# Kernel optimization log

Hardware: AMD Instinct MI355X
Metric: run time of the kernel (lower is better)

Reference implementation:

```python
import jax, jax.numpy as jnp
import numpy as np

INPUT, HIDDEN, CLASSES = 4096, 4096, 1000


def setup_inputs() -> dict:
    key = jax.random.key(0)
    kx, kw1, kb1, kw2, kb2 = jax.random.split(key, 5)
    return {
        "x": jax.random.normal(kx, (8192, INPUT), dtype=jnp.float32),
        "fc1_weight": jax.random.normal(kw1, (HIDDEN, INPUT), dtype=jnp.float32),
        "fc1_bias": jax.random.normal(kb1, (HIDDEN,), dtype=jnp.float32),
        "fc2_weight": jax.random.normal(kw2, (CLASSES, HIDDEN), dtype=jnp.float32),
        "fc2_bias": jax.random.normal(kb2, (CLASSES,), dtype=jnp.float32),
    }


def reference(x, fc1_weight, fc1_bias, fc2_weight, fc2_bias):
    # x: [B, INPUT] (module flattens; already flat here)
    hidden = jnp.einsum("bi,hi->bh", x, fc1_weight) + fc1_bias  # [B, H]
    activated = jax.nn.relu(hidden)
    logits = jnp.einsum("bh,ch->bc", activated, fc2_weight) + fc2_bias  # [B, C]
    return jax.nn.softmax(logits, axis=-1)
```

## Files before the change

kernel.cpp:

```cpp
#include <hip/hip_runtime.h>
#include <hip/hip_fp16.h>
#include <stdint.h>

typedef __attribute__((ext_vector_type(8)))  _Float16 f16x8;
typedef __attribute__((ext_vector_type(4)))  _Float16 f16x4;
typedef __attribute__((ext_vector_type(4)))  float    f32x4;

__device__ __forceinline__ void split4(const f32x4 v, f16x4 &h, f16x4 &l) {
    #pragma unroll
    for (int i = 0; i < 4; ++i) {
        float a = v[i];
        _Float16 hh = (_Float16)a;
        h[i] = hh;
        l[i] = (_Float16)(a - (float)hh);
    }
}

__global__ __launch_bounds__(256)
void split_rows(const float* __restrict__ src, _Float16* __restrict__ h,
                _Float16* __restrict__ l, int srcRows, long long total4)
{
    const long long stride = (long long)gridDim.x * blockDim.x;
    for (long long i = (long long)blockIdx.x * blockDim.x + threadIdx.x; i < total4; i += stride) {
        const long long e = i << 2;
        const int row = (int)(e >> 12);
        f16x4 hv = {}, lv = {};
        if (row < srcRows) {
            f32x4 v = *(const f32x4*)(src + e);
            split4(v, hv, lv);
        }
        *(f16x4*)(h + e) = hv;
        *(f16x4*)(l + e) = lv;
    }
}


#define BARRIER() __builtin_amdgcn_s_barrier()
#define SB0()     __builtin_amdgcn_sched_barrier(0)
#define MFMA16    __builtin_amdgcn_mfma_f32_16x16x32_f16
#define SGB       __builtin_amdgcn_sched_group_barrier

template<int N> __device__ __forceinline__ void VMCNT() {
    asm volatile("s_waitcnt vmcnt(%0)" :: "n"(N) : "memory");
    __builtin_amdgcn_sched_barrier(0);
}

__device__ __forceinline__ void gload16(const _Float16* g, _Float16* l) {
    __builtin_amdgcn_global_load_lds(
        (const __attribute__((address_space(1))) void*)g,
        (__attribute__((address_space(3))) void*)l, 16, 0, 0);
}

template<int MI, bool SPLITOUT, bool CHUNKSWZ>
__global__ __launch_bounds__(512, 2)
void gemm3_v9(const _Float16* __restrict__ Agh, const _Float16* __restrict__ Agl,
              const _Float16* __restrict__ Bgh, const _Float16* __restrict__ Bgl,
              const float* __restrict__ bias,
              _Float16* __restrict__ Oh, _Float16* __restrict__ Ol,
              float* __restrict__ Of, int ldo, int Nstore,
              int K, int nBN)
{
    extern __shared__ _Float16 lds[];
    constexpr int WROWS = MI * 16;
    constexpr int BM    = MI * 32;
    constexpr int CHA   = MI * 2;
    constexpr int PW    = (2*CHA + 32) / 8;
    constexpr int H1    = PW - CHA/8;
    constexpr int H2    = CHA / 8;
    constexpr int ALO   = CHA * 512;
    constexpr int BHO   = 2 * CHA * 512;
    constexpr int BUFS  = 2*CHA*512 + 16384;

    const int tid  = threadIdx.x;
    const int lane = tid & 63;
    const int wave = tid >> 6;
    const int wm = wave >> 2;
    const int wn = wave & 3;
    const int fr = lane & 15;
    const int fg = lane >> 4;

    int bm, bn;
    const int orig = blockIdx.x;
    if (CHUNKSWZ) {
        bm = ((orig & 7) << 2) | ((orig >> 3) & 3);
        bn = orig >> 5;
    } else {
        const int cpx  = gridDim.x >> 3;
        const int swzb = (orig & 7) * cpx + (orig >> 3);
        bn = swzb % nBN;
        bm = swzb / nBN;
    }
    const int m0 = bm * BM;
    const int n0 = bn * 256;

    const _Float16* gptr[8];
    int loff[8];
    #pragma unroll
    for (int i = 0; i < PW; ++i) {
        int p, q;
        if (i < H2 || i >= H1) {
            const bool hi = (i >= H1);
            const int  s  = hi ? (i - H1) : i;
            const int  j  = wave * H2 + s;
            p = j / (CHA / 2);
            const int v   = j % (CHA / 2);
            const int wmq = v / (MI / 2);
            const int wi  = v % (MI / 2);
            q = wmq * MI + (hi ? MI / 2 : 0) + wi;
        } else {
            q = (i - H2) + (wave & 3) * 4;
            p = 2 + (wave >> 2);
        }
        const int row = q*16 + (lane >> 2);
        const int gc  = (lane & 3) ^ ((row >> 1) & 3);
        const _Float16* plane = (p == 0) ? Agh : (p == 1) ? Agl : (p == 2) ? Bgh : Bgl;
        const size_t grow = (size_t)((p < 2) ? m0 : n0) + row;
        gptr[i] = plane + grow * (size_t)K + gc * 8;
        loff[i] = ((p < 2) ? p * ALO : BHO + (p - 2) * 8192) + q * 512;
    }

    const int swz8 = (fg ^ ((fr >> 1) & 3)) * 8;
    int aoff[MI], boff[4];
    #pragma unroll
    for (int mi = 0; mi < MI; ++mi) aoff[mi] = (wm*WROWS + mi*16 + fr)*32 + swz8;
    #pragma unroll
    for (int ni = 0; ni < 4; ++ni)  boff[ni] = BHO + (wn*64 + ni*16 + fr)*32 + swz8;

    f32x4 acc[MI][4] = {};

    #pragma unroll
    for (int i = 0; i < PW; ++i) { gload16(gptr[i], &lds[loff[i]]); gptr[i] += 32; }
    VMCNT<0>(); BARRIER(); SB0();

    const int NT = K >> 5;
    int bb = 0;

#define MFMA3(NI, AH, AL) do {                                           \
        acc[0][NI] = MFMA16((AH), bh##NI, acc[0][NI], 0, 0, 0);          \
        acc[0][NI] = MFMA16((AH), bl##NI, acc[0][NI], 0, 0, 0);          \
        acc[0][NI] = MFMA16((AL), bh##NI, acc[0][NI], 0, 0, 0);          \
    } while (0)

#define MFMA12(MIdx, AH, AL) do {                                        \
        acc[MIdx][0] = MFMA16((AH), bh0, acc[MIdx][0], 0, 0, 0);         \
        acc[MIdx][1] = MFMA16((AH), bh1, acc[MIdx][1], 0, 0, 0);         \
        acc[MIdx][2] = MFMA16((AH), bh2, acc[MIdx][2], 0, 0, 0);         \
        acc[MIdx][3] = MFMA16((AH), bh3, acc[MIdx][3], 0, 0, 0);         \
        acc[MIdx][0] = MFMA16((AH), bl0, acc[MIdx][0], 0, 0, 0);         \
        acc[MIdx][1] = MFMA16((AH), bl1, acc[MIdx][1], 0, 0, 0);         \
        acc[MIdx][2] = MFMA16((AH), bl2, acc[MIdx][2], 0, 0, 0);         \
        acc[MIdx][3] = MFMA16((AH), bl3, acc[MIdx][3], 0, 0, 0);         \
        acc[MIdx][0] = MFMA16((AL), bh0, acc[MIdx][0], 0, 0, 0);         \
        acc[MIdx][1] = MFMA16((AL), bh1, acc[MIdx][1], 0, 0, 0);         \
        acc[MIdx][2] = MFMA16((AL), bh2, acc[MIdx][2], 0, 0, 0);         \
        acc[MIdx][3] = MFMA16((AL), bh3, acc[MIdx][3], 0, 0, 0);         \
    } while (0)

#define STEP_BODY(STG)                                                            \
    do {                                                                          \
        if (STG) {                                                                \
            _Pragma("unroll")                                                     \
            for (int i = 0; i < PW; ++i) {                                        \
                gload16(gptr[i], &lds[nbuf + loff[i]]); gptr[i] += 32;            \
            }                                                                     \
        }                                                                         \
        f16x8 ah[2], al[2];                                                       \
        f16x8 bh0, bl0, bh1, bl1, bh2, bl2, bh3, bl3;                             \
        ah[0] = *(const f16x8*)&lds[bb + aoff[0]];                                \
        al[0] = *(const f16x8*)&lds[bb + ALO + aoff[0]];                          \
        bh0 = *(const f16x8*)&lds[bb + boff[0]];                                  \
        bl0 = *(const f16x8*)&lds[bb + 8192 + boff[0]];                           \
        if (STG) SGB(0x010, PW, 0);                                               \
        SGB(0x100, 4, 0);                                                         \
        MFMA3(0, ah[0], al[0]);                                                   \
        SGB(0x008, 3, 0);                                                         \
        bh1 = *(const f16x8*)&lds[bb + boff[1]];                                  \
        bl1 = *(const f16x8*)&lds[bb + 8192 + boff[1]];                           \
        SGB(0x100, 2, 0);                                                         \
        MFMA3(1, ah[0], al[0]);                                                   \
        SGB(0x008, 3, 0);                                                         \
        bh2 = *(const f16x8*)&lds[bb + boff[2]];                                  \
        bl2 = *(const f16x8*)&lds[bb + 8192 + boff[2]];                           \
        SGB(0x100, 2, 0);                                                         \
        MFMA3(2, ah[0], al[0]);                                                   \
        SGB(0x008, 3, 0);                                                         \
        bh3 = *(const f16x8*)&lds[bb + boff[3]];                                  \
        bl3 = *(const f16x8*)&lds[bb + 8192 + boff[3]];                           \
        ah[1] = *(const f16x8*)&lds[bb + aoff[1]];                                \
        al[1] = *(const f16x8*)&lds[bb + ALO + aoff[1]];                          \
        SGB(0x100, 4, 0);                                                         \
        MFMA3(3, ah[0], al[0]);                                                   \
        SGB(0x008, 3, 0);                                                         \
        _Pragma("unroll")                                                         \
        for (int mi = 1; mi < MI; ++mi) {                                         \
            if (mi < MI - 1) {                                                    \
                ah[(mi + 1) & 1] = *(const f16x8*)&lds[bb + aoff[mi + 1]];        \
                al[(mi + 1) & 1] = *(const f16x8*)&lds[bb + ALO + aoff[mi + 1]];  \
                SGB(0x100, 2, 0);                                                 \
            }                                                                     \
            MFMA12(mi, ah[mi & 1], al[mi & 1]);                                   \
            SGB(0x008, 12, 0);                                                    \
        }                                                                         \
    } while (0)

    for (int t = 0; t < NT - 1; ++t) {
        const int nbuf = BUFS - bb;
        STEP_BODY(true);
        VMCNT<0>(); BARRIER(); SB0();
        bb = nbuf;
    }
    {
        const int nbuf = 0; (void)nbuf;
        STEP_BODY(false);
    }
#undef STEP_BODY
#undef MFMA12
#undef MFMA3

    #pragma unroll
    for (int ni = 0; ni < 4; ++ni) {
        const int n = n0 + wn*64 + ni*16 + fr;
        if (!SPLITOUT && n >= Nstore) continue;
        const float bv = bias[n];
        #pragma unroll
        for (int mi = 0; mi < MI; ++mi) {
            #pragma unroll
            for (int j = 0; j < 4; ++j) {
                const int m = m0 + wm*WROWS + mi*16 + fg*4 + j;
                float v = acc[mi][ni][j] + bv;
                if (SPLITOUT) {
                    v = fmaxf(v, 0.f);
                    const _Float16 hh = (_Float16)v;
                    Oh[(size_t)m * ldo + n] = hh;
                    Ol[(size_t)m * ldo + n] = (_Float16)(v - (float)hh);
                } else {
                    Of[(size_t)m * ldo + n] = v;
                }
            }
        }
    }
}

#define TILE_M 128
#define TILE_N 128
#define TILE_K 32
#define LDSK   40

template<bool RELU, bool NGUARD>
__global__ __launch_bounds__(256, 2)
void gemm_split3(const float* __restrict__ A, const float* __restrict__ B,
                 const float* __restrict__ bias, float* __restrict__ C,
                 int K, int ldc, int Nreal)
{
    __shared__ _Float16 Ah[TILE_M][LDSK];
    __shared__ _Float16 Al[TILE_M][LDSK];
    __shared__ _Float16 Bh[TILE_N][LDSK];
    __shared__ _Float16 Bl[TILE_N][LDSK];

    const int tid  = threadIdx.x;
    const int lane = tid & 63;
    const int wave = tid >> 6;
    const int wr   = wave >> 1;
    const int wc   = wave & 1;
    const int m0   = blockIdx.x * TILE_M;
    const int n0   = blockIdx.y * TILE_N;
    const int srow = tid >> 3;
    const int scol = (tid & 7) << 2;
    const int fr = lane & 15;
    const int fg = lane >> 4;

    f32x4 acc[4][4] = {};

    for (int kt = 0; kt < K; kt += TILE_K) {
        __syncthreads();
        #pragma unroll
        for (int p = 0; p < 4; ++p) {
            const int row = srow + p * 32;
            f32x4 v = *(const f32x4*)(A + (size_t)(m0 + row) * K + kt + scol);
            f16x4 hv, lv;
            split4(v, hv, lv);
            *(f16x4*)&Ah[row][scol] = hv;
            *(f16x4*)&Al[row][scol] = lv;
        }
        #pragma unroll
        for (int p = 0; p < 4; ++p) {
            const int row = srow + p * 32;
            f32x4 v = {0.f, 0.f, 0.f, 0.f};
            if (!NGUARD || (n0 + row) < Nreal)
                v = *(const f32x4*)(B + (size_t)(n0 + row) * K + kt + scol);
            f16x4 hv, lv;
            split4(v, hv, lv);
            *(f16x4*)&Bh[row][scol] = hv;
            *(f16x4*)&Bl[row][scol] = lv;
        }
        __syncthreads();

        f16x8 ah[4], al[4];
        #pragma unroll
        for (int mi = 0; mi < 4; ++mi) {
            const int r = wr * 64 + mi * 16 + fr;
            ah[mi] = *(const f16x8*)&Ah[r][fg * 8];
            al[mi] = *(const f16x8*)&Al[r][fg * 8];
        }
        #pragma unroll
        for (int ni = 0; ni < 4; ++ni) {
            const int r = wc * 64 + ni * 16 + fr;
            const f16x8 bh = *(const f16x8*)&Bh[r][fg * 8];
            const f16x8 bl = *(const f16x8*)&Bl[r][fg * 8];
            #pragma unroll
            for (int mi = 0; mi < 4; ++mi) {
                acc[mi][ni] = __builtin_amdgcn_mfma_f32_16x16x32_f16(ah[mi], bh, acc[mi][ni], 0, 0, 0);
                acc[mi][ni] = __builtin_amdgcn_mfma_f32_16x16x32_f16(ah[mi], bl, acc[mi][ni], 0, 0, 0);
                acc[mi][ni] = __builtin_amdgcn_mfma_f32_16x16x32_f16(al[mi], bh, acc[mi][ni], 0, 0, 0);
            }
        }
    }

    #pragma unroll
    for (int ni = 0; ni < 4; ++ni) {
        const int n = n0 + wc * 64 + ni * 16 + fr;
        if (NGUARD && n >= Nreal) continue;
        const float bv = bias[n];
        #pragma unroll
        for (int mi = 0; mi < 4; ++mi) {
            #pragma unroll
            for (int j = 0; j < 4; ++j) {
                const int m = m0 + wr * 64 + mi * 16 + fg * 4 + j;
                float val = acc[mi][ni][j] + bv;
                if (RELU) val = fmaxf(val, 0.f);
                C[(size_t)m * ldc + n] = val;
            }
        }
    }
}

__global__ __launch_bounds__(256)
void softmax_rows(float* __restrict__ out, int rows, int cols)
{
    const int lane = threadIdx.x & 63;
    const int row  = blockIdx.x * 4 + (threadIdx.x >> 6);
    if (row >= rows) return;
    float* p = out + (size_t)row * cols;

    float v[16];
    float mx = -3.4e38f;
    #pragma unroll
    for (int j = 0; j < 16; ++j) {
        const int c = lane + j * 64;
        v[j] = (c < cols) ? p[c] : -3.4e38f;
        mx = fmaxf(mx, v[j]);
    }
    #pragma unroll
    for (int off = 32; off > 0; off >>= 1)
        mx = fmaxf(mx, __shfl_xor(mx, off));

    float s = 0.f;
    #pragma unroll
    for (int j = 0; j < 16; ++j) {
        const int c = lane + j * 64;
        const float e = (c < cols) ? __expf(v[j] - mx) : 0.f;
        v[j] = e;
        s += e;
    }
    #pragma unroll
    for (int off = 32; off > 0; off >>= 1)
        s += __shfl_xor(s, off);

    const float inv = 1.f / s;
    #pragma unroll
    for (int j = 0; j < 16; ++j) {
        const int c = lane + j * 64;
        if (c < cols) p[c] = v[j] * inv;
    }
}

extern "C" void kernel_launch(void* const* d_in, const int* in_sizes, int n_in,
                              void* d_out, int out_size, void* d_ws, size_t ws_size,
                              hipStream_t stream)
{
    const float* x  = (const float*)d_in[0];
    const float* w1 = (const float*)d_in[1];
    const float* b1 = (const float*)d_in[2];
    const float* w2 = (const float*)d_in[3];
    const float* b2 = (const float*)d_in[4];
    float* out = (float*)d_out;

    const size_t SZ_X  = (size_t)8192 * 4096 * 2;
    const size_t SZ_W1 = (size_t)4096 * 4096 * 2;
    const size_t SZ_W2 = (size_t)1024 * 4096 * 2;

    size_t off = 0;
    auto take = [&](size_t b) { size_t o = off; off += (b + 255) & ~(size_t)255; return o; };
    const size_t o_xh  = take(SZ_X),  o_xl  = take(SZ_X);
    const size_t o_w1h = take(SZ_W1), o_w1l = take(SZ_W1);
    const size_t o_w2h = take(SZ_W2), o_w2l = take(SZ_W2);
    const size_t o_ah  = take(SZ_X),  o_al  = take(SZ_X);
    const size_t need = off;

    bool attr_ok =
        (hipFuncSetAttribute((const void*)gemm3_v9<8, true, true>,
                             hipFuncAttributeMaxDynamicSharedMemorySize, 131072) == hipSuccess) &&
        (hipFuncSetAttribute((const void*)gemm3_v9<4, false, false>,
                             hipFuncAttributeMaxDynamicSharedMemorySize, 131072) == hipSuccess);

    const dim3 blk256(256, 1, 1), blk512(512, 1, 1);

    if (attr_ok && ws_size >= need) {
        char* w = (char*)d_ws;
        _Float16 *xh  = (_Float16*)(w + o_xh),  *xl  = (_Float16*)(w + o_xl);
        _Float16 *w1h = (_Float16*)(w + o_w1h), *w1l = (_Float16*)(w + o_w1l);
        _Float16 *w2h = (_Float16*)(w + o_w2h), *w2l = (_Float16*)(w + o_w2l);
        _Float16 *ath = (_Float16*)(w + o_ah),  *atl = (_Float16*)(w + o_al);

        hipLaunchKernelGGL(split_rows, dim3(2048), blk256, 0, stream, x,  xh,  xl,  8192, (long long)8192 * 1024);
        hipLaunchKernelGGL(split_rows, dim3(2048), blk256, 0, stream, w1, w1h, w1l, 4096, (long long)4096 * 1024);
        hipLaunchKernelGGL(split_rows, dim3(1024), blk256, 0, stream, w2, w2h, w2l, 1000, (long long)1024 * 1024);

        hipLaunchKernelGGL((gemm3_v9<8, true, true>), dim3(512), blk512, 131072, stream,
                           xh, xl, w1h, w1l, b1, ath, atl, (float*)nullptr, 4096, 4096, 4096, 16);
        hipLaunchKernelGGL((gemm3_v9<4, false, false>), dim3(256), blk512, 98304, stream,
                           ath, atl, w2h, w2l, b2, (_Float16*)nullptr, (_Float16*)nullptr,
                           out, 1000, 1000, 4096, 4);
        hipLaunchKernelGGL(softmax_rows, dim3(2048), blk256, 0, stream, out, 8192, 1000);
    } else {
        float* act = (float*)d_ws;
        hipLaunchKernelGGL((gemm_split3<true, false>), dim3(64, 32), blk256, 0, stream,
                           x, w1, b1, act, 4096, 4096, 4096);
        hipLaunchKernelGGL((gemm_split3<false, true>), dim3(64, 8), blk256, 0, stream,
                           act, w2, b2, out, 4096, 1000, 1000);
        hipLaunchKernelGGL(softmax_rows, dim3(2048), blk256, 0, stream, out, 8192, 1000);
    }
}
```

Before: 953.5 us.

## Shrink GEMM block tile to 128x128 with smaller LDS for higher occupancy

```diff
diff --git a/kernel.cpp b/kernel.cpp
--- a/kernel.cpp
+++ b/kernel.cpp
@@ -51,25 +51,20 @@
         (__attribute__((address_space(3))) void*)l, 16, 0, 0);
 }
 
-template<int MI, bool SPLITOUT, bool CHUNKSWZ>
-__global__ __launch_bounds__(512, 2)
-void gemm3_v9(const _Float16* __restrict__ Agh, const _Float16* __restrict__ Agl,
-              const _Float16* __restrict__ Bgh, const _Float16* __restrict__ Bgl,
-              const float* __restrict__ bias,
-              _Float16* __restrict__ Oh, _Float16* __restrict__ Ol,
-              float* __restrict__ Of, int ldo, int Nstore,
-              int K, int nBN)
+template<bool SPLITOUT>
+__global__ __launch_bounds__(512, 4)
+void gemm3_v10(const _Float16* __restrict__ Agh, const _Float16* __restrict__ Agl,
+               const _Float16* __restrict__ Bgh, const _Float16* __restrict__ Bgl,
+               const float* __restrict__ bias,
+               _Float16* __restrict__ Oh, _Float16* __restrict__ Ol,
+               float* __restrict__ Of, int ldo, int Nstore,
+               int K)
 {
     extern __shared__ _Float16 lds[];
-    constexpr int WROWS = MI * 16;
-    constexpr int BM    = MI * 32;
-    constexpr int CHA   = MI * 2;
-    constexpr int PW    = (2*CHA + 32) / 8;
-    constexpr int H1    = PW - CHA/8;
-    constexpr int H2    = CHA / 8;
-    constexpr int ALO   = CHA * 512;
-    constexpr int BHO   = 2 * CHA * 512;
-    constexpr int BUFS  = 2*CHA*512 + 16384;
+    constexpr int PW   = 4;
+    constexpr int ALO  = 4096;
+    constexpr int BHO  = 8192;
+    constexpr int BUFS = 16384;
 
     const int tid  = threadIdx.x;
     const int lane = tid & 63;
@@ -79,54 +74,35 @@
     const int fr = lane & 15;
     const int fg = lane >> 4;
 
-    int bm, bn;
     const int orig = blockIdx.x;
-    if (CHUNKSWZ) {
-        bm = ((orig & 7) << 2) | ((orig >> 3) & 3);
-        bn = orig >> 5;
-    } else {
-        const int cpx  = gridDim.x >> 3;
-        const int swzb = (orig & 7) * cpx + (orig >> 3);
-        bn = swzb % nBN;
-        bm = swzb / nBN;
-    }
-    const int m0 = bm * BM;
-    const int n0 = bn * 256;
-
-    const _Float16* gptr[8];
-    int loff[8];
+    const int bm = ((orig & 7) << 3) | ((orig >> 3) & 7);
+    const int bn = orig >> 6;
+    const int m0 = bm * 128;
+    const int n0 = bn * 128;
+
+    const _Float16* gptr[PW];
+    int loff[PW];
     #pragma unroll
     for (int i = 0; i < PW; ++i) {
-        int p, q;
-        if (i < H2 || i >= H1) {
-            const bool hi = (i >= H1);
-            const int  s  = hi ? (i - H1) : i;
-            const int  j  = wave * H2 + s;
-            p = j / (CHA / 2);
-            const int v   = j % (CHA / 2);
-            const int wmq = v / (MI / 2);
-            const int wi  = v % (MI / 2);
-            q = wmq * MI + (hi ? MI / 2 : 0) + wi;
-        } else {
-            q = (i - H2) + (wave & 3) * 4;
-            p = 2 + (wave >> 2);
-        }
+        const int c = wave * PW + i;
+        const int p = c >> 3;
+        const int q = c & 7;
         const int row = q*16 + (lane >> 2);
         const int gc  = (lane & 3) ^ ((row >> 1) & 3);
         const _Float16* plane = (p == 0) ? Agh : (p == 1) ? Agl : (p == 2) ? Bgh : Bgl;
         const size_t grow = (size_t)((p < 2) ? m0 : n0) + row;
         gptr[i] = plane + grow * (size_t)K + gc * 8;
-        loff[i] = ((p < 2) ? p * ALO : BHO + (p - 2) * 8192) + q * 512;
+        loff[i] = p * 4096 + q * 512;
     }
 
     const int swz8 = (fg ^ ((fr >> 1) & 3)) * 8;
-    int aoff[MI], boff[4];
-    #pragma unroll
-    for (int mi = 0; mi < MI; ++mi) aoff[mi] = (wm*WROWS + mi*16 + fr)*32 + swz8;
-    #pragma unroll
-    for (int ni = 0; ni < 4; ++ni)  boff[ni] = BHO + (wn*64 + ni*16 + fr)*32 + swz8;
-
-    f32x4 acc[MI][4] = {};
+    int aoff[4], boff[2];
+    #pragma unroll
+    for (int mi = 0; mi < 4; ++mi) aoff[mi] = (wm*64 + mi*16 + fr)*32 + swz8;
+    #pragma unroll
+    for (int ni = 0; ni < 2; ++ni)  boff[ni] = BHO + (wn*32 + ni*16 + fr)*32 + swz8;
+
+    f32x4 acc[4][2] = {};
 
     #pragma unroll
     for (int i = 0; i < PW; ++i) { gload16(gptr[i], &lds[loff[i]]); gptr[i] += 32; }
@@ -135,25 +111,10 @@
     const int NT = K >> 5;
     int bb = 0;
 
-#define MFMA3(NI, AH, AL) do {                                           \
-        acc[0][NI] = MFMA16((AH), bh##NI, acc[0][NI], 0, 0, 0);          \
-        acc[0][NI] = MFMA16((AH), bl##NI, acc[0][NI], 0, 0, 0);          \
-        acc[0][NI] = MFMA16((AL), bh##NI, acc[0][NI], 0, 0, 0);          \
-    } while (0)
-
-#define MFMA12(MIdx, AH, AL) do {                                        \
-        acc[MIdx][0] = MFMA16((AH), bh0, acc[MIdx][0], 0, 0, 0);         \
-        acc[MIdx][1] = MFMA16((AH), bh1, acc[MIdx][1], 0, 0, 0);         \
-        acc[MIdx][2] = MFMA16((AH), bh2, acc[MIdx][2], 0, 0, 0);         \
-        acc[MIdx][3] = MFMA16((AH), bh3, acc[MIdx][3], 0, 0, 0);         \
-        acc[MIdx][0] = MFMA16((AH), bl0, acc[MIdx][0], 0, 0, 0);         \
-        acc[MIdx][1] = MFMA16((AH), bl1, acc[MIdx][1], 0, 0, 0);         \
-        acc[MIdx][2] = MFMA16((AH), bl2, acc[MIdx][2], 0, 0, 0);         \
-        acc[MIdx][3] = MFMA16((AH), bl3, acc[MIdx][3], 0, 0, 0);         \
-        acc[MIdx][0] = MFMA16((AL), bh0, acc[MIdx][0], 0, 0, 0);         \
-        acc[MIdx][1] = MFMA16((AL), bh1, acc[MIdx][1], 0, 0, 0);         \
-        acc[MIdx][2] = MFMA16((AL), bh2, acc[MIdx][2], 0, 0, 0);         \
-        acc[MIdx][3] = MFMA16((AL), bh3, acc[MIdx][3], 0, 0, 0);         \
+#define MFMA3(MIdx, NIdx, AH, AL, BH, BL) do {                               \
+        acc[MIdx][NIdx] = MFMA16((AH), (BH), acc[MIdx][NIdx], 0, 0, 0);      \
+        acc[MIdx][NIdx] = MFMA16((AH), (BL), acc[MIdx][NIdx], 0, 0, 0);      \
+        acc[MIdx][NIdx] = MFMA16((AL), (BH), acc[MIdx][NIdx], 0, 0, 0);      \
     } while (0)
 
 #define STEP_BODY(STG)                                                            \
@@ -165,41 +126,33 @@
             }                                                                     \
         }                                                                         \
         f16x8 ah[2], al[2];                                                       \
-        f16x8 bh0, bl0, bh1, bl1, bh2, bl2, bh3, bl3;                             \
+        f16x8 bh0, bl0, bh1, bl1;                                                 \
         ah[0] = *(const f16x8*)&lds[bb + aoff[0]];                                \
         al[0] = *(const f16x8*)&lds[bb + ALO + aoff[0]];                          \
         bh0 = *(const f16x8*)&lds[bb + boff[0]];                                  \
-        bl0 = *(const f16x8*)&lds[bb + 8192 + boff[0]];                           \
+        bl0 = *(const f16x8*)&lds[bb + 4096 + boff[0]];                           \
         if (STG) SGB(0x010, PW, 0);                                               \
         SGB(0x100, 4, 0);                                                         \
-        MFMA3(0, ah[0], al[0]);                                                   \
+        MFMA3(0, 0, ah[0], al[0], bh0, bl0);                                      \
         SGB(0x008, 3, 0);                                                         \
         bh1 = *(const f16x8*)&lds[bb + boff[1]];                                  \
-        bl1 = *(const f16x8*)&lds[bb + 8192 + boff[1]];                           \
+        bl1 = *(const f16x8*)&lds[bb + 4096 + boff[1]];                           \
         SGB(0x100, 2, 0);                                                         \
-        MFMA3(1, ah[0], al[0]);                                                   \
+        MFMA3(0, 1, ah[0], al[0], bh1, bl1);                                      \
         SGB(0x008, 3, 0);                                                         \
-        bh2 = *(const f16x8*)&lds[bb + boff[2]];                                  \
-        bl2 = *(const f16x8*)&lds[bb + 8192 + boff[2]];                           \
-        SGB(0x100, 2, 0);                                                         \
-        MFMA3(2, ah[0], al[0]);                                                   \
-        SGB(0x008, 3, 0);                                                         \
-        bh3 = *(const f16x8*)&lds[bb + boff[3]];                                  \
-        bl3 = *(const f16x8*)&lds[bb + 8192 + boff[3]];                           \
         ah[1] = *(const f16x8*)&lds[bb + aoff[1]];                                \
         al[1] = *(const f16x8*)&lds[bb + ALO + aoff[1]];                          \
-        SGB(0x100, 4, 0);                                                         \
-        MFMA3(3, ah[0], al[0]);                                                   \
-        SGB(0x008, 3, 0);                                                         \
+        SGB(0x100, 2, 0);                                                         \
         _Pragma("unroll")                                                         \
-        for (int mi = 1; mi < MI; ++mi) {                                         \
-            if (mi < MI - 1) {                                                    \
+        for (int mi = 1; mi < 4; ++mi) {                                          \
+            if (mi < 3) {                                                         \
                 ah[(mi + 1) & 1] = *(const f16x8*)&lds[bb + aoff[mi + 1]];        \
                 al[(mi + 1) & 1] = *(const f16x8*)&lds[bb + ALO + aoff[mi + 1]];  \
                 SGB(0x100, 2, 0);                                                 \
             }                                                                     \
-            MFMA12(mi, ah[mi & 1], al[mi & 1]);                                   \
-            SGB(0x008, 12, 0);                                                    \
+            MFMA3(mi, 0, ah[mi & 1], al[mi & 1], bh0, bl0);                       \
+            MFMA3(mi, 1, ah[mi & 1], al[mi & 1], bh1, bl1);                       \
+            SGB(0x008, 6, 0);                                                     \
         }                                                                         \
     } while (0)
 
@@ -214,19 +167,18 @@
         STEP_BODY(false);
     }
 #undef STEP_BODY
-#undef MFMA12
 #undef MFMA3
 
     #pragma unroll
-    for (int ni = 0; ni < 4; ++ni) {
-        const int n = n0 + wn*64 + ni*16 + fr;
+    for (int ni = 0; ni < 2; ++ni) {
+        const int n = n0 + wn*32 + ni*16 + fr;
         if (!SPLITOUT && n >= Nstore) continue;
         const float bv = bias[n];
         #pragma unroll
-        for (int mi = 0; mi < MI; ++mi) {
+        for (int mi = 0; mi < 4; ++mi) {
             #pragma unroll
             for (int j = 0; j < 4; ++j) {
-                const int m = m0 + wm*WROWS + mi*16 + fg*4 + j;
+                const int m = m0 + wm*64 + mi*16 + fg*4 + j;
                 float v = acc[mi][ni][j] + bv;
                 if (SPLITOUT) {
                     v = fmaxf(v, 0.f);
@@ -398,10 +350,10 @@
     const size_t need = off;
 
     bool attr_ok =
-        (hipFuncSetAttribute((const void*)gemm3_v9<8, true, true>,
-                             hipFuncAttributeMaxDynamicSharedMemorySize, 131072) == hipSuccess) &&
-        (hipFuncSetAttribute((const void*)gemm3_v9<4, false, false>,
-                             hipFuncAttributeMaxDynamicSharedMemorySize, 131072) == hipSuccess);
+        (hipFuncSetAttribute((const void*)gemm3_v10<true>,
+                             hipFuncAttributeMaxDynamicSharedMemorySize, 65536) == hipSuccess) &&
+        (hipFuncSetAttribute((const void*)gemm3_v10<false>,
+                             hipFuncAttributeMaxDynamicSharedMemorySize, 65536) == hipSuccess);
 
     const dim3 blk256(256, 1, 1), blk512(512, 1, 1);
 
@@ -416,11 +368,11 @@
         hipLaunchKernelGGL(split_rows, dim3(2048), blk256, 0, stream, w1, w1h, w1l, 4096, (long long)4096 * 1024);
         hipLaunchKernelGGL(split_rows, dim3(1024), blk256, 0, stream, w2, w2h, w2l, 1000, (long long)1024 * 1024);
 
-        hipLaunchKernelGGL((gemm3_v9<8, true, true>), dim3(512), blk512, 131072, stream,
-                           xh, xl, w1h, w1l, b1, ath, atl, (float*)nullptr, 4096, 4096, 4096, 16);
-        hipLaunchKernelGGL((gemm3_v9<4, false, false>), dim3(256), blk512, 98304, stream,
+        hipLaunchKernelGGL((gemm3_v10<true>), dim3(2048), blk512, 65536, stream,
+                           xh, xl, w1h, w1l, b1, ath, atl, (float*)nullptr, 4096, 4096, 4096);
+        hipLaunchKernelGGL((gemm3_v10<false>), dim3(512), blk512, 65536, stream,
                            ath, atl, w2h, w2l, b2, (_Float16*)nullptr, (_Float16*)nullptr,
-                           out, 1000, 1000, 4096, 4);
+                           out, 1000, 1000, 4096);
         hipLaunchKernelGGL(softmax_rows, dim3(2048), blk256, 0, stream, out, 8192, 1000);
     } else {
         float* act = (float*)d_ws;
```

New measurement: 1.017 ms. +6.7%, slower.
